# Kernel optimization log

Hardware: AMD Instinct MI355X
Metric: run time of the kernel (lower is better)

The kernel has to match this reference:

```python
import jax, jax.numpy as jnp
import numpy as np

DIM = 1024
HEADS = 16
HEAD_DIM = DIM // HEADS
B, N = 2, 2048


def setup_inputs() -> dict:
    key = jax.random.key(0)
    k1, k2, k3, k4 = jax.random.split(key, 4)
    scale = 1.0 / np.sqrt(DIM)
    return {
        "x": jax.random.normal(k1, (B, N, DIM), dtype=jnp.float32),
        "w_qkv": jax.random.normal(k2, (DIM, 3 * DIM), dtype=jnp.float32) * scale,
        "w_out": jax.random.normal(k3, (DIM, DIM), dtype=jnp.float32) * scale,
        "b_out": jax.random.normal(k4, (DIM,), dtype=jnp.float32) * 0.01,
    }


def reference(x, w_qkv, w_out, b_out):
    b, n, c = x.shape
    h, d = HEADS, c // HEADS
    sm_scale = d ** -0.5
    qkv = x @ w_qkv  # [b, n, 3c]
    q, k, v = jnp.split(qkv, 3, axis=-1)
    # [b, n, c] -> [b, h, n, d]
    q = q.reshape(b, n, h, d).transpose(0, 2, 1, 3)
    k = k.reshape(b, n, h, d).transpose(0, 2, 1, 3)
    v = v.reshape(b, n, h, d).transpose(0, 2, 1, 3)
    dots = jnp.einsum("bhqd,bhkd->bhqk", q, k) * sm_scale
    attn = jax.nn.softmax(dots, axis=-1)
    out = jnp.einsum("bhqk,bhkd->bhqd", attn, v)
    out = out.transpose(0, 2, 1, 3).reshape(b, n, c)
    return out @ w_out + b_out
```

## Files before the change

### kernel.cpp

```cpp
#include <hip/hip_runtime.h>
#include <hip/hip_bf16.h>

typedef __attribute__((ext_vector_type(8))) short bf16x8;
typedef __attribute__((ext_vector_type(4))) float f32x4;

#define B_    2
#define N_    2048
#define DIM_  1024
#define H_    16
#define D_    64
#define BH_   32
#define QSC   0.18033688f

static __device__ __forceinline__ void gload_lds16(const void* g, void* l) {
  __builtin_amdgcn_global_load_lds((const __attribute__((address_space(1))) void*)g,
                                   (__attribute__((address_space(3))) void*)l, 16, 0, 0);
}

__global__ __launch_bounds__(256) void prep_kernel(const float* __restrict__ x,
                                                   const float* __restrict__ w_qkv,
                                                   const float* __restrict__ w_out,
                                                   __hip_bfloat16* __restrict__ xb,
                                                   __hip_bfloat16* __restrict__ wqkT,
                                                   __hip_bfloat16* __restrict__ woT) {
  __shared__ float tile[64][65];
  const int bid = blockIdx.x, t = threadIdx.x;
  if (bid < 4096) {
    const int i = bid * 256 + t;
    float4 v = reinterpret_cast<const float4*>(x)[i];
    union { __hip_bfloat16 h[4]; uint2 u; } cv;
    cv.h[0] = __float2bfloat16(v.x);
    cv.h[1] = __float2bfloat16(v.y);
    cv.h[2] = __float2bfloat16(v.z);
    cv.h[3] = __float2bfloat16(v.w);
    reinterpret_cast<uint2*>(xb)[i] = cv.u;
    return;
  }
  const float* in;
  __hip_bfloat16* out;
  int R, C, c0, r0;
  if (bid < 4096 + 768) {
    const int bx = bid - 4096;
    in = w_qkv; out = wqkT; R = 1024; C = 3072;
    c0 = (bx % 48) * 64; r0 = (bx / 48) * 64;
  } else {
    const int bx = bid - 4096 - 768;
    in = w_out; out = woT; R = 1024; C = 1024;
    c0 = (bx % 16) * 64; r0 = (bx / 16) * 64;
  }
#pragma unroll
  for (int i = 0; i < 16; ++i) {
    int idx = i * 256 + t;
    int r = idx >> 6, c = idx & 63;
    tile[r][c] = in[(size_t)(r0 + r) * C + (c0 + c)];
  }
  __syncthreads();
#pragma unroll
  for (int i = 0; i < 16; ++i) {
    int idx = i * 256 + t;
    int rr = idx >> 6, cc = idx & 63;
    out[(size_t)(c0 + rr) * R + (r0 + cc)] = __float2bfloat16(tile[cc][rr]);
  }
}

__global__ __launch_bounds__(512, 2) void gemm_qkv_kernel(const __hip_bfloat16* __restrict__ A,
                                                          const __hip_bfloat16* __restrict__ Bt,
                                                          __hip_bfloat16* __restrict__ Qw,
                                                          __hip_bfloat16* __restrict__ Kw,
                                                          __hip_bfloat16* __restrict__ Vt) {
  __shared__ __align__(16) char lds[131072];
  const int t = threadIdx.x, w = t >> 6, lane = t & 63;
  const int l16 = lane & 15, kg = lane >> 4;
  int flat = blockIdx.y * 12 + blockIdx.x;
  flat = (flat & 7) * 24 + (flat >> 3);
  const int bx = flat % 12, by = flat / 12;
  const int m0 = by * 256, n0 = bx * 256;
  const int wm = w >> 2, wn = w & 3;
  const int rA = t >> 3;
  const int jb = (t & 7) ^ (rA & 7);

#define LDSOFF(bb, mat) (((bb) * 2 + (mat)) * 32768)
#define STG_A(bb, tt, h)                                                                    \
  do {                                                                                      \
    gload_lds16(A + (size_t)(m0 + rA + 64 * (h)) * 1024 + (tt) * 64 + jb * 8,               \
                (char*)lds + LDSOFF(bb, 0) + (h) * 8192 + t * 16);                          \
    gload_lds16(A + (size_t)(m0 + rA + 64 * (h) + 128) * 1024 + (tt) * 64 + jb * 8,         \
                (char*)lds + LDSOFF(bb, 0) + (h) * 8192 + 16384 + t * 16);                  \
  } while (0)
#define STG_B(bb, tt, h)                                                                    \
  do {                                                                                      \
    gload_lds16(Bt + (size_t)(n0 + rA + 128 * (h)) * 1024 + (tt) * 64 + jb * 8,             \
                (char*)lds + LDSOFF(bb, 1) + (h) * 16384 + t * 16);                         \
    gload_lds16(Bt + (size_t)(n0 + rA + 128 * (h) + 64) * 1024 + (tt) * 64 + jb * 8,        \
                (char*)lds + LDSOFF(bb, 1) + (h) * 16384 + 8192 + t * 16);                  \
  } while (0)
#define RD_A(dst, q, i, kk)                                                                 \
  {                                                                                         \
    const int row = wm * 128 + ((q) * 2 + (i)) * 16 + l16;                                  \
    dst = *reinterpret_cast<const bf16x8*>(Ab + row * 128 + ((((kk) * 4 + kg) ^ (row & 7)) * 16)); \
  }
#define RD_B(dst, nj, kk)                                                                   \
  {                                                                                         \
    const int row = wn * 64 + (nj) * 16 + l16;                                              \
    dst = *reinterpret_cast<const bf16x8*>(Bb + row * 128 + ((((kk) * 4 + kg) ^ (row & 7)) * 16)); \
  }
#define PHASE(q)                                                                            \
  do {                                                                                      \
    bf16x8 af[2][2];                                                                        \
    _Pragma("unroll") for (int i = 0; i < 2; ++i)                                           \
      _Pragma("unroll") for (int kk = 0; kk < 2; ++kk) RD_A(af[i][kk], q, i, kk);           \
    __builtin_amdgcn_s_setprio(1);                                                          \
    _Pragma("unroll") for (int i = 0; i < 2; ++i)                                           \
      _Pragma("unroll") for (int nj = 0; nj < 4; ++nj)                                      \
        _Pragma("unroll") for (int kk = 0; kk < 2; ++kk)                                    \
          acc[(q) * 2 + i][nj] =                                                            \
              __builtin_amdgcn_mfma_f32_16x16x32_bf16(af[i][kk], bfr[nj][kk],               \
                                                      acc[(q) * 2 + i][nj], 0, 0, 0);       \
    __builtin_amdgcn_s_setprio(0);                                                          \
  } while (0)

  f32x4 acc[8][4];
#pragma unroll
  for (int i = 0; i < 8; ++i)
#pragma unroll
    for (int j = 0; j < 4; ++j) acc[i][j] = {0.f, 0.f, 0.f, 0.f};

  STG_A(0, 0, 0); STG_A(0, 0, 1); STG_B(0, 0, 0); STG_B(0, 0, 1);
  STG_B(1, 1, 0); STG_B(1, 1, 1); STG_A(1, 1, 0);

#pragma unroll 1
  for (int kt = 0; kt < 16; ++kt) {
    const int b = kt & 1;
    const char* Ab = (const char*)lds + LDSOFF(b, 0);
    const char* Bb = (const char*)lds + LDSOFF(b, 1);

    if (kt < 15) STG_A(b ^ 1, kt + 1, 1);
    __builtin_amdgcn_sched_barrier(0);
    if (kt < 15) asm volatile("s_waitcnt vmcnt(8)" ::: "memory");
    else         asm volatile("s_waitcnt vmcnt(0)" ::: "memory");
    __builtin_amdgcn_s_barrier();
    __builtin_amdgcn_sched_barrier(0);
    bf16x8 bfr[4][2];
#pragma unroll
    for (int nj = 0; nj < 4; ++nj)
#pragma unroll
      for (int kk = 0; kk < 2; ++kk) RD_B(bfr[nj][kk], nj, kk);
    PHASE(0);
    __builtin_amdgcn_s_barrier();
    __builtin_amdgcn_sched_barrier(0);

    if (kt < 14) STG_B(b, kt + 2, 0);
    __builtin_amdgcn_sched_barrier(0);
    PHASE(1);
    __builtin_amdgcn_s_barrier();
    __builtin_amdgcn_sched_barrier(0);

    if (kt < 14) STG_B(b, kt + 2, 1);
    PHASE(2);

    if (kt < 14) STG_A(b, kt + 2, 0);
    __builtin_amdgcn_sched_barrier(0);
    PHASE(3);
    __builtin_amdgcn_s_barrier();
    __builtin_amdgcn_sched_barrier(0);
  }

  const int which = n0 >> 10;
#pragma unroll
  for (int nj = 0; nj < 4; ++nj) {
    const int n = n0 + wn * 64 + nj * 16 + l16;
    const int nn = n & 1023;
    const int h = nn >> 6, d = nn & 63;
#pragma unroll
    for (int mi = 0; mi < 8; ++mi) {
      const int m = m0 + wm * 128 + mi * 16 + kg * 4;
      const int bb = m >> 11, tt = m & 2047;
      if (which == 2) {
        union { __hip_bfloat16 hh[4]; unsigned long long u; } pv;
#pragma unroll
        for (int r = 0; r < 4; ++r) pv.hh[r] = __float2bfloat16(acc[mi][nj][r]);
        *reinterpret_cast<unsigned long long*>(
            &Vt[((size_t)(bb * H_ + h) * D_ + d) * N_ + tt]) = pv.u;
      } else {
        __hip_bfloat16* dst = (which == 0) ? Qw : Kw;
        const float sc = (which == 0) ? QSC : 1.0f;
#pragma unroll
        for (int r = 0; r < 4; ++r)
          dst[((size_t)(bb * H_ + h) * N_ + tt + r) * D_ + d] = __float2bfloat16(acc[mi][nj][r] * sc);
      }
    }
  }
#undef PHASE
#undef RD_B
#undef RD_A
#undef STG_B
#undef STG_A
#undef LDSOFF
}

__global__ __launch_bounds__(256) void gemm_out_kernel(const __hip_bfloat16* __restrict__ A,
                                                       const __hip_bfloat16* __restrict__ Bt,
                                                       const float* __restrict__ bo,
                                                       float* __restrict__ out) {
  __shared__ __align__(16) char lds[65536];
  const int t = threadIdx.x, w = t >> 6, lane = t & 63;
  const int l16 = lane & 15, kg = lane >> 4;
  const int m0 = blockIdx.y * 128, n0 = blockIdx.x * 128;
  const int wm = w >> 1, wn = w & 1;

  f32x4 acc[4][4];
#pragma unroll
  for (int i = 0; i < 4; ++i)
#pragma unroll
    for (int j = 0; j < 4; ++j) acc[i][j] = {0.f, 0.f, 0.f, 0.f};

  size_t srcA[4], srcB[4];
#pragma unroll
  for (int i = 0; i < 4; ++i) {
    const int c = 256 * i + t;
    const int row = c >> 3, jsw = (c & 7) ^ (row & 7);
    srcA[i] = (size_t)(m0 + row) * 1024 + jsw * 8;
    srcB[i] = (size_t)(n0 + row) * 1024 + jsw * 8;
  }
#define OSTG(bb, k0)                                                          \
  do {                                                                        \
    _Pragma("unroll") for (int i = 0; i < 4; ++i) {                           \
      gload_lds16(A + srcA[i] + (k0), (char*)lds + (bb) * 32768 + i * 4096 + w * 1024);          \
      gload_lds16(Bt + srcB[i] + (k0), (char*)lds + (bb) * 32768 + 16384 + i * 4096 + w * 1024); \
    }                                                                         \
  } while (0)

  OSTG(0, 0);

#pragma unroll 1
  for (int kt = 0; kt < 16; ++kt) {
    const int b = kt & 1;
    __builtin_amdgcn_s_barrier();
    __builtin_amdgcn_sched_barrier(0);
    if (kt + 1 < 16) OSTG(b ^ 1, (kt + 1) * 64);
    __builtin_amdgcn_sched_barrier(0);
    if (kt + 1 < 16) asm volatile("s_waitcnt vmcnt(8)" ::: "memory");
    else             asm volatile("s_waitcnt vmcnt(0)" ::: "memory");
    __builtin_amdgcn_s_barrier();
    __builtin_amdgcn_sched_barrier(0);
    const char* Ab = (const char*)lds + b * 32768;
    const char* Bb = (const char*)lds + b * 32768 + 16384;
#pragma unroll
    for (int kk = 0; kk < 2; ++kk) {
      bf16x8 a[4], bfr[4];
#pragma unroll
      for (int i = 0; i < 4; ++i) {
        const int row = wm * 64 + i * 16 + l16;
        const int jsw = ((kk << 2) | kg) ^ (row & 7);
        a[i] = *reinterpret_cast<const bf16x8*>(Ab + row * 128 + jsw * 16);
      }
#pragma unroll
      for (int j = 0; j < 4; ++j) {
        const int row = wn * 64 + j * 16 + l16;
        const int jsw = ((kk << 2) | kg) ^ (row & 7);
        bfr[j] = *reinterpret_cast<const bf16x8*>(Bb + row * 128 + jsw * 16);
      }
      __builtin_amdgcn_s_setprio(1);
#pragma unroll
      for (int i = 0; i < 4; ++i)
#pragma unroll
        for (int j = 0; j < 4; ++j)
          acc[i][j] = __builtin_amdgcn_mfma_f32_16x16x32_bf16(a[i], bfr[j], acc[i][j], 0, 0, 0);
      __builtin_amdgcn_s_setprio(0);
    }
  }
#undef OSTG

#pragma unroll
  for (int j = 0; j < 4; ++j) {
    const int n = n0 + wn * 64 + j * 16 + l16;
    const float bias = bo[n];
#pragma unroll
    for (int i = 0; i < 4; ++i) {
#pragma unroll
      for (int r = 0; r < 4; ++r) {
        const int m = m0 + wm * 64 + i * 16 + kg * 4 + r;
        out[(size_t)m * 1024 + n] = acc[i][j][r] + bias;
      }
    }
  }
}

__global__ __launch_bounds__(512) void attn_kernel(const __hip_bfloat16* __restrict__ Q,
                                                   const __hip_bfloat16* __restrict__ K,
                                                   const __hip_bfloat16* __restrict__ Vt,
                                                   __hip_bfloat16* __restrict__ O) {
  __shared__ __align__(16) __hip_bfloat16 Ks[3][64 * 64];
  __shared__ __align__(16) __hip_bfloat16 Vs[3][64 * 64];
  __shared__ __align__(16) __hip_bfloat16 Plds[8][16][64];
  const int bh = blockIdx.y;
  const int q0 = blockIdx.x * 128;
  const int t = threadIdx.x, w = t >> 6, lane = t & 63;
  const int l16 = lane & 15, kg = lane >> 4;
  const int b = bh >> 4, h = bh & 15;

  const __hip_bfloat16* Kbh = K + (size_t)bh * N_ * D_;
  const __hip_bfloat16* Vbh = Vt + (size_t)bh * D_ * N_;

  const int crow = t >> 3, cb = t & 7;
  const int csw = cb ^ (crow & 7);
  const size_t offK = (size_t)crow * D_ + csw * 8;
  const size_t offV = (size_t)crow * N_ + csw * 8;

  const __hip_bfloat16* Qp = Q + ((size_t)bh * N_ + q0 + w * 16 + l16) * D_ + kg * 8;
  const bf16x8 qf0 = *reinterpret_cast<const bf16x8*>(Qp);
  const bf16x8 qf1 = *reinterpret_cast<const bf16x8*>(Qp + 32);

  float dacc = 0.f;
  f32x4 oacc[4];
#pragma unroll
  for (int dn = 0; dn < 4; ++dn) oacc[dn] = {0.f, 0.f, 0.f, 0.f};

#define STAGE(bufi, kv)                                                          \
  do {                                                                           \
    gload_lds16(Kbh + (size_t)(kv) * D_ + offK, (char*)Ks[bufi] + w * 1024);     \
    gload_lds16(Vbh + (kv) + offV,              (char*)Vs[bufi] + w * 1024);     \
  } while (0)

  STAGE(0, 0);
  STAGE(1, 64);

#pragma unroll 1
  for (int it = 0; it < N_ / 64; ++it) {
    if (it < N_ / 64 - 1) asm volatile("s_waitcnt vmcnt(2)" ::: "memory");
    else                  asm volatile("s_waitcnt vmcnt(0)" ::: "memory");
    __builtin_amdgcn_s_barrier();
    __builtin_amdgcn_sched_barrier(0);
    if (it + 2 < N_ / 64) STAGE((it + 2) % 3, (it + 2) * 64);
    __builtin_amdgcn_sched_barrier(0);

    const char* Kb = (const char*)Ks[it % 3];
    const char* Vb = (const char*)Vs[it % 3];

    f32x4 s[4];
#pragma unroll
    for (int kt = 0; kt < 4; ++kt) s[kt] = {0.f, 0.f, 0.f, 0.f};
    __builtin_amdgcn_s_setprio(1);
#pragma unroll
    for (int kt = 0; kt < 4; ++kt) {
      const int row = kt * 16 + l16;
      const int rsw = (row & 7) << 4;
      const bf16x8 k0 = *reinterpret_cast<const bf16x8*>(Kb + row * 128 + ((kg << 4) ^ rsw));
      const bf16x8 k1 = *reinterpret_cast<const bf16x8*>(Kb + row * 128 + (((4 + kg) << 4) ^ rsw));
      s[kt] = __builtin_amdgcn_mfma_f32_16x16x32_bf16(k0, qf0, s[kt], 0, 0, 0);
      s[kt] = __builtin_amdgcn_mfma_f32_16x16x32_bf16(k1, qf1, s[kt], 0, 0, 0);
    }
    __builtin_amdgcn_s_setprio(0);

    const int xm3 = (l16 & 7) << 3;
    float ds = 0.f;
#pragma unroll
    for (int kt = 0; kt < 4; ++kt) {
      const float p0 = __builtin_amdgcn_exp2f(s[kt][0]);
      const float p1 = __builtin_amdgcn_exp2f(s[kt][1]);
      const float p2 = __builtin_amdgcn_exp2f(s[kt][2]);
      const float p3 = __builtin_amdgcn_exp2f(s[kt][3]);
      ds += (p0 + p1) + (p2 + p3);
      union { __hip_bfloat162 h2[2]; unsigned long long u; } pk;
      pk.h2[0] = __float22bfloat162_rn(make_float2(p0, p1));
      pk.h2[1] = __float22bfloat162_rn(make_float2(p2, p3));
      *reinterpret_cast<unsigned long long*>(&Plds[w][l16][(16 * kt + 4 * kg) ^ xm3]) = pk.u;
    }
    dacc += ds;

    __builtin_amdgcn_s_setprio(1);
#pragma unroll
    for (int kk = 0; kk < 2; ++kk) {
      const bf16x8 pa = *reinterpret_cast<const bf16x8*>(
          &Plds[w][l16][(kk * 32 + kg * 8) ^ xm3]);
#pragma unroll
      for (int dn = 0; dn < 4; ++dn) {
        const int vrow = dn * 16 + l16;
        const int vsw = (vrow & 7) << 4;
        const bf16x8 vf = *reinterpret_cast<const bf16x8*>(
            Vb + vrow * 128 + ((kk * 64 + kg * 16) ^ vsw));
        oacc[dn] = __builtin_amdgcn_mfma_f32_16x16x32_bf16(pa, vf, oacc[dn], 0, 0, 0);
      }
    }
    __builtin_amdgcn_s_setprio(0);
  }
#undef STAGE

  float dtot = dacc + __shfl_xor(dacc, 16);
  dtot += __shfl_xor(dtot, 32);
  float inv[4];
#pragma unroll
  for (int r = 0; r < 4; ++r) inv[r] = 1.0f / __shfl(dtot, kg * 4 + r);

  __hip_bfloat16* Ob = O + ((size_t)b * N_ + q0 + w * 16) * DIM_ + h * D_;
#pragma unroll
  for (int dn = 0; dn < 4; ++dn)
#pragma unroll
    for (int r = 0; r < 4; ++r)
      Ob[(size_t)(kg * 4 + r) * DIM_ + dn * 16 + l16] = __float2bfloat16(oacc[dn][r] * inv[r]);
}

extern "C" void kernel_launch(void* const* d_in, const int* in_sizes, int n_in,
                              void* d_out, int out_size, void* d_ws, size_t ws_size,
                              hipStream_t stream) {
  const float* x = (const float*)d_in[0];
  const float* w_qkv = (const float*)d_in[1];
  const float* w_out = (const float*)d_in[2];
  const float* b_out = (const float*)d_in[3];
  float* out = (float*)d_out;

  __hip_bfloat16* ws = (__hip_bfloat16*)d_ws;
  __hip_bfloat16* xb = ws;
  __hip_bfloat16* wqkT = xb + (size_t)4096 * 1024;
  __hip_bfloat16* woT = wqkT + (size_t)3072 * 1024;
  __hip_bfloat16* Qw = woT + (size_t)1024 * 1024;
  __hip_bfloat16* Kw = Qw + (size_t)BH_ * N_ * D_;
  __hip_bfloat16* Vt = Kw + (size_t)BH_ * N_ * D_;
  __hip_bfloat16* Ow = Vt + (size_t)BH_ * N_ * D_;

  prep_kernel<<<5120, 256, 0, stream>>>(x, w_qkv, w_out, xb, wqkT, woT);
  gemm_qkv_kernel<<<dim3(12, 16), 512, 0, stream>>>(xb, wqkT, Qw, Kw, Vt);
  attn_kernel<<<dim3(16, 32), 512, 0, stream>>>(Qw, Kw, Vt, Ow);
  gemm_out_kernel<<<dim3(8, 32), 256, 0, stream>>>(Ow, woT, b_out, out);
}
```

Before: 116.3 us.

## Split attention KV loop across two wave groups with 32-row Q per wave

Each wave now handles 32 query rows, so every K fragment read from LDS feeds two Q tiles. The eight waves split into two groups that process alternating KV tiles out of a four-deep LDS ring, and their partial outputs are merged through LDS at the end. The softmax denominator is now computed with an MFMA against a ones vector instead of scalar adds plus shuffles. This adds an end-of-kernel reduction, a larger LDS footprint that may limit occupancy, and a full vmcnt(0) wait on every iteration.

```diff
diff --git a/kernel.cpp b/kernel.cpp
--- a/kernel.cpp
+++ b/kernel.cpp
@@ -286,18 +286,18 @@
   }
 }
 
-__global__ __launch_bounds__(512) void attn_kernel(const __hip_bfloat16* __restrict__ Q,
-                                                   const __hip_bfloat16* __restrict__ K,
-                                                   const __hip_bfloat16* __restrict__ Vt,
-                                                   __hip_bfloat16* __restrict__ O) {
-  __shared__ __align__(16) __hip_bfloat16 Ks[3][64 * 64];
-  __shared__ __align__(16) __hip_bfloat16 Vs[3][64 * 64];
-  __shared__ __align__(16) __hip_bfloat16 Plds[8][16][64];
+__global__ __launch_bounds__(512, 4) void attn_kernel(const __hip_bfloat16* __restrict__ Q,
+                                                      const __hip_bfloat16* __restrict__ K,
+                                                      const __hip_bfloat16* __restrict__ Vt,
+                                                      __hip_bfloat16* __restrict__ O) {
+  __shared__ __align__(16) char lds[81920];
   const int bh = blockIdx.y;
   const int q0 = blockIdx.x * 128;
   const int t = threadIdx.x, w = t >> 6, lane = t & 63;
   const int l16 = lane & 15, kg = lane >> 4;
   const int b = bh >> 4, h = bh & 15;
+  const int grp = w >> 2;
+  const int qbase = q0 + (w & 3) * 32;
 
   const __hip_bfloat16* Kbh = K + (size_t)bh * N_ * D_;
   const __hip_bfloat16* Vbh = Vt + (size_t)bh * D_ * N_;
@@ -307,39 +307,58 @@
   const size_t offK = (size_t)crow * D_ + csw * 8;
   const size_t offV = (size_t)crow * N_ + csw * 8;
 
-  const __hip_bfloat16* Qp = Q + ((size_t)bh * N_ + q0 + w * 16 + l16) * D_ + kg * 8;
-  const bf16x8 qf0 = *reinterpret_cast<const bf16x8*>(Qp);
-  const bf16x8 qf1 = *reinterpret_cast<const bf16x8*>(Qp + 32);
-
-  float dacc = 0.f;
-  f32x4 oacc[4];
-#pragma unroll
-  for (int dn = 0; dn < 4; ++dn) oacc[dn] = {0.f, 0.f, 0.f, 0.f};
-
-#define STAGE(bufi, kv)                                                          \
-  do {                                                                           \
-    gload_lds16(Kbh + (size_t)(kv) * D_ + offK, (char*)Ks[bufi] + w * 1024);     \
-    gload_lds16(Vbh + (kv) + offV,              (char*)Vs[bufi] + w * 1024);     \
+  bf16x8 qf[2][2];
+#pragma unroll
+  for (int qh = 0; qh < 2; ++qh) {
+    const __hip_bfloat16* Qrow = Q + ((size_t)bh * N_ + qbase + 16 * qh + l16) * D_ + kg * 8;
+    qf[qh][0] = *reinterpret_cast<const bf16x8*>(Qrow);
+    qf[qh][1] = *reinterpret_cast<const bf16x8*>(Qrow + 32);
+  }
+
+  bf16x8 ones;
+#pragma unroll
+  for (int i = 0; i < 8; ++i) ones[i] = (short)0x3F80;
+
+  f32x4 oaccS[2];
+  f32x4 oacc[2][4];
+#pragma unroll
+  for (int qh = 0; qh < 2; ++qh) {
+    oaccS[qh] = {0.f, 0.f, 0.f, 0.f};
+#pragma unroll
+    for (int dn = 0; dn < 4; ++dn) oacc[qh][dn] = {0.f, 0.f, 0.f, 0.f};
+  }
+
+  char* Plw = lds + 65536 + w * 2048;
+
+#define STAGE(bufi, kv)                                                            \
+  do {                                                                             \
+    gload_lds16(Kbh + (size_t)(kv) * D_ + offK, lds + (bufi) * 16384 + w * 1024);  \
+    gload_lds16(Vbh + (kv) + offV, lds + (bufi) * 16384 + 8192 + w * 1024);        \
   } while (0)
 
   STAGE(0, 0);
   STAGE(1, 64);
 
 #pragma unroll 1
-  for (int it = 0; it < N_ / 64; ++it) {
-    if (it < N_ / 64 - 1) asm volatile("s_waitcnt vmcnt(2)" ::: "memory");
-    else                  asm volatile("s_waitcnt vmcnt(0)" ::: "memory");
-    __builtin_amdgcn_s_barrier();
-    __builtin_amdgcn_sched_barrier(0);
-    if (it + 2 < N_ / 64) STAGE((it + 2) % 3, (it + 2) * 64);
-    __builtin_amdgcn_sched_barrier(0);
-
-    const char* Kb = (const char*)Ks[it % 3];
-    const char* Vb = (const char*)Vs[it % 3];
-
-    f32x4 s[4];
-#pragma unroll
-    for (int kt = 0; kt < 4; ++kt) s[kt] = {0.f, 0.f, 0.f, 0.f};
+  for (int p = 0; p < 16; ++p) {
+    asm volatile("s_waitcnt vmcnt(0)" ::: "memory");
+    __builtin_amdgcn_s_barrier();
+    __builtin_amdgcn_sched_barrier(0);
+    if (p < 15) {
+      STAGE((2 * p + 2) & 3, (2 * p + 2) * 64);
+      STAGE((2 * p + 3) & 3, (2 * p + 3) * 64);
+    }
+    __builtin_amdgcn_sched_barrier(0);
+
+    const int myt = 2 * p + grp;
+    const char* Kb = lds + (myt & 3) * 16384;
+    const char* Vb = Kb + 8192;
+
+    f32x4 s[2][4];
+#pragma unroll
+    for (int qh = 0; qh < 2; ++qh)
+#pragma unroll
+      for (int kt = 0; kt < 4; ++kt) s[qh][kt] = {0.f, 0.f, 0.f, 0.f};
     __builtin_amdgcn_s_setprio(1);
 #pragma unroll
     for (int kt = 0; kt < 4; ++kt) {
@@ -347,57 +366,81 @@
       const int rsw = (row & 7) << 4;
       const bf16x8 k0 = *reinterpret_cast<const bf16x8*>(Kb + row * 128 + ((kg << 4) ^ rsw));
       const bf16x8 k1 = *reinterpret_cast<const bf16x8*>(Kb + row * 128 + (((4 + kg) << 4) ^ rsw));
-      s[kt] = __builtin_amdgcn_mfma_f32_16x16x32_bf16(k0, qf0, s[kt], 0, 0, 0);
-      s[kt] = __builtin_amdgcn_mfma_f32_16x16x32_bf16(k1, qf1, s[kt], 0, 0, 0);
+      s[0][kt] = __builtin_amdgcn_mfma_f32_16x16x32_bf16(k0, qf[0][0], s[0][kt], 0, 0, 0);
+      s[0][kt] = __builtin_amdgcn_mfma_f32_16x16x32_bf16(k1, qf[0][1], s[0][kt], 0, 0, 0);
+      s[1][kt] = __builtin_amdgcn_mfma_f32_16x16x32_bf16(k0, qf[1][0], s[1][kt], 0, 0, 0);
+      s[1][kt] = __builtin_amdgcn_mfma_f32_16x16x32_bf16(k1, qf[1][1], s[1][kt], 0, 0, 0);
     }
     __builtin_amdgcn_s_setprio(0);
 
     const int xm3 = (l16 & 7) << 3;
-    float ds = 0.f;
-#pragma unroll
-    for (int kt = 0; kt < 4; ++kt) {
-      const float p0 = __builtin_amdgcn_exp2f(s[kt][0]);
-      const float p1 = __builtin_amdgcn_exp2f(s[kt][1]);
-      const float p2 = __builtin_amdgcn_exp2f(s[kt][2]);
-      const float p3 = __builtin_amdgcn_exp2f(s[kt][3]);
-      ds += (p0 + p1) + (p2 + p3);
-      union { __hip_bfloat162 h2[2]; unsigned long long u; } pk;
-      pk.h2[0] = __float22bfloat162_rn(make_float2(p0, p1));
-      pk.h2[1] = __float22bfloat162_rn(make_float2(p2, p3));
-      *reinterpret_cast<unsigned long long*>(&Plds[w][l16][(16 * kt + 4 * kg) ^ xm3]) = pk.u;
-    }
-    dacc += ds;
-
-    __builtin_amdgcn_s_setprio(1);
-#pragma unroll
-    for (int kk = 0; kk < 2; ++kk) {
-      const bf16x8 pa = *reinterpret_cast<const bf16x8*>(
-          &Plds[w][l16][(kk * 32 + kg * 8) ^ xm3]);
-#pragma unroll
-      for (int dn = 0; dn < 4; ++dn) {
-        const int vrow = dn * 16 + l16;
-        const int vsw = (vrow & 7) << 4;
-        const bf16x8 vf = *reinterpret_cast<const bf16x8*>(
-            Vb + vrow * 128 + ((kk * 64 + kg * 16) ^ vsw));
-        oacc[dn] = __builtin_amdgcn_mfma_f32_16x16x32_bf16(pa, vf, oacc[dn], 0, 0, 0);
-      }
-    }
-    __builtin_amdgcn_s_setprio(0);
+#pragma unroll
+    for (int qh = 0; qh < 2; ++qh) {
+#pragma unroll
+      for (int kt = 0; kt < 4; ++kt) {
+        union { __hip_bfloat162 h2[2]; unsigned long long u; } pk;
+        pk.h2[0] = __float22bfloat162_rn(make_float2(__builtin_amdgcn_exp2f(s[qh][kt][0]),
+                                                     __builtin_amdgcn_exp2f(s[qh][kt][1])));
+        pk.h2[1] = __float22bfloat162_rn(make_float2(__builtin_amdgcn_exp2f(s[qh][kt][2]),
+                                                     __builtin_amdgcn_exp2f(s[qh][kt][3])));
+        *reinterpret_cast<unsigned long long*>(
+            Plw + l16 * 128 + ((16 * kt + 4 * kg) ^ xm3) * 2) = pk.u;
+      }
+      __builtin_amdgcn_s_setprio(1);
+#pragma unroll
+      for (int kk = 0; kk < 2; ++kk) {
+        const bf16x8 pa = *reinterpret_cast<const bf16x8*>(
+            Plw + l16 * 128 + ((kk * 32 + kg * 8) ^ xm3) * 2);
+        oaccS[qh] = __builtin_amdgcn_mfma_f32_16x16x32_bf16(pa, ones, oaccS[qh], 0, 0, 0);
+#pragma unroll
+        for (int dn = 0; dn < 4; ++dn) {
+          const int vrow = dn * 16 + l16;
+          const int vsw = (vrow & 7) << 4;
+          const bf16x8 vf = *reinterpret_cast<const bf16x8*>(
+              Vb + vrow * 128 + ((kk * 64 + kg * 16) ^ vsw));
+          oacc[qh][dn] = __builtin_amdgcn_mfma_f32_16x16x32_bf16(pa, vf, oacc[qh][dn], 0, 0, 0);
+        }
+      }
+      __builtin_amdgcn_s_setprio(0);
+      __builtin_amdgcn_sched_barrier(0);
+    }
   }
 #undef STAGE
 
-  float dtot = dacc + __shfl_xor(dacc, 16);
-  dtot += __shfl_xor(dtot, 32);
-  float inv[4];
-#pragma unroll
-  for (int r = 0; r < 4; ++r) inv[r] = 1.0f / __shfl(dtot, kg * 4 + r);
-
-  __hip_bfloat16* Ob = O + ((size_t)b * N_ + q0 + w * 16) * DIM_ + h * D_;
-#pragma unroll
-  for (int dn = 0; dn < 4; ++dn)
-#pragma unroll
-    for (int r = 0; r < 4; ++r)
-      Ob[(size_t)(kg * 4 + r) * DIM_ + dn * 16 + l16] = __float2bfloat16(oacc[dn][r] * inv[r]);
+  __syncthreads();
+  float* red = (float*)lds;
+  if (grp == 1) {
+    const int wp = w - 4;
+#pragma unroll
+    for (int qh = 0; qh < 2; ++qh) {
+#pragma unroll
+      for (int dn = 0; dn < 4; ++dn)
+#pragma unroll
+        for (int r = 0; r < 4; ++r)
+          red[(qh * 16 + dn * 4 + r) * 256 + wp * 64 + lane] = oacc[qh][dn][r];
+#pragma unroll
+      for (int r = 0; r < 4; ++r)
+        red[(32 + qh * 4 + r) * 256 + wp * 64 + lane] = oaccS[qh][r];
+    }
+  }
+  __syncthreads();
+  if (grp == 0) {
+#pragma unroll
+    for (int qh = 0; qh < 2; ++qh) {
+      float inv[4];
+#pragma unroll
+      for (int r = 0; r < 4; ++r)
+        inv[r] = 1.0f / (oaccS[qh][r] + red[(32 + qh * 4 + r) * 256 + w * 64 + lane]);
+      __hip_bfloat16* Ob = O + ((size_t)b * N_ + qbase + 16 * qh) * DIM_ + h * D_;
+#pragma unroll
+      for (int dn = 0; dn < 4; ++dn)
+#pragma unroll
+        for (int r = 0; r < 4; ++r) {
+          const float v = (oacc[qh][dn][r] + red[(qh * 16 + dn * 4 + r) * 256 + w * 64 + lane]) * inv[r];
+          Ob[(size_t)(kg * 4 + r) * DIM_ + dn * 16 + l16] = __float2bfloat16(v);
+        }
+    }
+  }
 }
 
 extern "C" void kernel_launch(void* const* d_in, const int* in_sizes, int n_in,
```

New measurement: 111.4 us. 1.04x faster.

## Process two KV tiles per barrier and compute softmax row sums with MFMA

Applied to the files above, without the earlier changes.

The attention loop now handles two 64-key tiles per iteration from a double-buffered 64 KB LDS region, replacing the three-stage single-tile ring. This halves the number of barriers and waitcnts per key. The softmax denominator is now accumulated by an MFMA of P against a ones vector instead of VALU adds and cross-lane shuffles, so the sum uses the same bf16-rounded P as the numerator. Launch bounds now request occupancy 4, which caps registers per thread; the larger 80 KB LDS footprint may limit how many blocks fit on each CU.

```diff
diff --git a/kernel.cpp b/kernel.cpp
--- a/kernel.cpp
+++ b/kernel.cpp
@@ -286,13 +286,11 @@
   }
 }
 
-__global__ __launch_bounds__(512) void attn_kernel(const __hip_bfloat16* __restrict__ Q,
-                                                   const __hip_bfloat16* __restrict__ K,
-                                                   const __hip_bfloat16* __restrict__ Vt,
-                                                   __hip_bfloat16* __restrict__ O) {
-  __shared__ __align__(16) __hip_bfloat16 Ks[3][64 * 64];
-  __shared__ __align__(16) __hip_bfloat16 Vs[3][64 * 64];
-  __shared__ __align__(16) __hip_bfloat16 Plds[8][16][64];
+__global__ __launch_bounds__(512, 4) void attn_kernel(const __hip_bfloat16* __restrict__ Q,
+                                                      const __hip_bfloat16* __restrict__ K,
+                                                      const __hip_bfloat16* __restrict__ Vt,
+                                                      __hip_bfloat16* __restrict__ O) {
+  __shared__ __align__(16) char lds[81920];
   const int bh = blockIdx.y;
   const int q0 = blockIdx.x * 128;
   const int t = threadIdx.x, w = t >> 6, lane = t & 63;
@@ -311,87 +309,128 @@
   const bf16x8 qf0 = *reinterpret_cast<const bf16x8*>(Qp);
   const bf16x8 qf1 = *reinterpret_cast<const bf16x8*>(Qp + 32);
 
-  float dacc = 0.f;
+  bf16x8 ones;
+#pragma unroll
+  for (int i = 0; i < 8; ++i) ones[i] = (short)0x3F80;
+
+  f32x4 oaccS = {0.f, 0.f, 0.f, 0.f};
   f32x4 oacc[4];
 #pragma unroll
   for (int dn = 0; dn < 4; ++dn) oacc[dn] = {0.f, 0.f, 0.f, 0.f};
 
-#define STAGE(bufi, kv)                                                          \
-  do {                                                                           \
-    gload_lds16(Kbh + (size_t)(kv) * D_ + offK, (char*)Ks[bufi] + w * 1024);     \
-    gload_lds16(Vbh + (kv) + offV,              (char*)Vs[bufi] + w * 1024);     \
-  } while (0)
-
-  STAGE(0, 0);
-  STAGE(1, 64);
+  char* Plw = lds + 65536 + w * 2048;
+
+#define STAGE1(base, kv)                                                \
+  do {                                                                  \
+    gload_lds16(Kbh + (size_t)(kv) * D_ + offK, (base) + w * 1024);     \
+    gload_lds16(Vbh + (kv) + offV, (base) + 8192 + w * 1024);           \
+  } while (0)
+#define STAGEP(pb, kv0)                                                 \
+  do {                                                                  \
+    STAGE1(lds + (pb) * 32768, kv0);                                    \
+    STAGE1(lds + (pb) * 32768 + 16384, (kv0) + 64);                     \
+  } while (0)
+
+  STAGEP(0, 0);
+  asm volatile("s_waitcnt vmcnt(0)" ::: "memory");
+  __builtin_amdgcn_s_barrier();
 
 #pragma unroll 1
-  for (int it = 0; it < N_ / 64; ++it) {
-    if (it < N_ / 64 - 1) asm volatile("s_waitcnt vmcnt(2)" ::: "memory");
-    else                  asm volatile("s_waitcnt vmcnt(0)" ::: "memory");
-    __builtin_amdgcn_s_barrier();
-    __builtin_amdgcn_sched_barrier(0);
-    if (it + 2 < N_ / 64) STAGE((it + 2) % 3, (it + 2) * 64);
-    __builtin_amdgcn_sched_barrier(0);
-
-    const char* Kb = (const char*)Ks[it % 3];
-    const char* Vb = (const char*)Vs[it % 3];
-
-    f32x4 s[4];
-#pragma unroll
-    for (int kt = 0; kt < 4; ++kt) s[kt] = {0.f, 0.f, 0.f, 0.f};
+  for (int p = 0; p < 16; ++p) {
+    if (p < 15) STAGEP((p + 1) & 1, (2 * p + 2) * 64);
+    __builtin_amdgcn_sched_barrier(0);
+
+    const char* base = lds + (p & 1) * 32768;
+    const char* Kb0 = base;
+    const char* Vb0 = base + 8192;
+    const char* Kb1 = base + 16384;
+    const char* Vb1 = base + 24576;
+
+    f32x4 s0[4], s1[4];
+#pragma unroll
+    for (int kt = 0; kt < 4; ++kt) { s0[kt] = {0.f, 0.f, 0.f, 0.f}; s1[kt] = {0.f, 0.f, 0.f, 0.f}; }
     __builtin_amdgcn_s_setprio(1);
 #pragma unroll
     for (int kt = 0; kt < 4; ++kt) {
       const int row = kt * 16 + l16;
       const int rsw = (row & 7) << 4;
-      const bf16x8 k0 = *reinterpret_cast<const bf16x8*>(Kb + row * 128 + ((kg << 4) ^ rsw));
-      const bf16x8 k1 = *reinterpret_cast<const bf16x8*>(Kb + row * 128 + (((4 + kg) << 4) ^ rsw));
-      s[kt] = __builtin_amdgcn_mfma_f32_16x16x32_bf16(k0, qf0, s[kt], 0, 0, 0);
-      s[kt] = __builtin_amdgcn_mfma_f32_16x16x32_bf16(k1, qf1, s[kt], 0, 0, 0);
+      const int o0 = (kg << 4) ^ rsw, o1 = ((4 + kg) << 4) ^ rsw;
+      const bf16x8 ka0 = *reinterpret_cast<const bf16x8*>(Kb0 + row * 128 + o0);
+      const bf16x8 ka1 = *reinterpret_cast<const bf16x8*>(Kb0 + row * 128 + o1);
+      const bf16x8 kb0 = *reinterpret_cast<const bf16x8*>(Kb1 + row * 128 + o0);
+      const bf16x8 kb1 = *reinterpret_cast<const bf16x8*>(Kb1 + row * 128 + o1);
+      s0[kt] = __builtin_amdgcn_mfma_f32_16x16x32_bf16(ka0, qf0, s0[kt], 0, 0, 0);
+      s0[kt] = __builtin_amdgcn_mfma_f32_16x16x32_bf16(ka1, qf1, s0[kt], 0, 0, 0);
+      s1[kt] = __builtin_amdgcn_mfma_f32_16x16x32_bf16(kb0, qf0, s1[kt], 0, 0, 0);
+      s1[kt] = __builtin_amdgcn_mfma_f32_16x16x32_bf16(kb1, qf1, s1[kt], 0, 0, 0);
     }
     __builtin_amdgcn_s_setprio(0);
 
     const int xm3 = (l16 & 7) << 3;
-    float ds = 0.f;
+
 #pragma unroll
     for (int kt = 0; kt < 4; ++kt) {
-      const float p0 = __builtin_amdgcn_exp2f(s[kt][0]);
-      const float p1 = __builtin_amdgcn_exp2f(s[kt][1]);
-      const float p2 = __builtin_amdgcn_exp2f(s[kt][2]);
-      const float p3 = __builtin_amdgcn_exp2f(s[kt][3]);
-      ds += (p0 + p1) + (p2 + p3);
       union { __hip_bfloat162 h2[2]; unsigned long long u; } pk;
-      pk.h2[0] = __float22bfloat162_rn(make_float2(p0, p1));
-      pk.h2[1] = __float22bfloat162_rn(make_float2(p2, p3));
-      *reinterpret_cast<unsigned long long*>(&Plds[w][l16][(16 * kt + 4 * kg) ^ xm3]) = pk.u;
-    }
-    dacc += ds;
-
+      pk.h2[0] = __float22bfloat162_rn(make_float2(__builtin_amdgcn_exp2f(s0[kt][0]),
+                                                   __builtin_amdgcn_exp2f(s0[kt][1])));
+      pk.h2[1] = __float22bfloat162_rn(make_float2(__builtin_amdgcn_exp2f(s0[kt][2]),
+                                                   __builtin_amdgcn_exp2f(s0[kt][3])));
+      *reinterpret_cast<unsigned long long*>(
+          Plw + l16 * 128 + (((16 * kt + 4 * kg) ^ xm3) << 1)) = pk.u;
+    }
     __builtin_amdgcn_s_setprio(1);
 #pragma unroll
     for (int kk = 0; kk < 2; ++kk) {
       const bf16x8 pa = *reinterpret_cast<const bf16x8*>(
-          &Plds[w][l16][(kk * 32 + kg * 8) ^ xm3]);
+          Plw + l16 * 128 + (((kk * 32 + kg * 8) ^ xm3) << 1));
+      oaccS = __builtin_amdgcn_mfma_f32_16x16x32_bf16(pa, ones, oaccS, 0, 0, 0);
 #pragma unroll
       for (int dn = 0; dn < 4; ++dn) {
         const int vrow = dn * 16 + l16;
         const int vsw = (vrow & 7) << 4;
         const bf16x8 vf = *reinterpret_cast<const bf16x8*>(
-            Vb + vrow * 128 + ((kk * 64 + kg * 16) ^ vsw));
+            Vb0 + vrow * 128 + ((kk * 64 + kg * 16) ^ vsw));
         oacc[dn] = __builtin_amdgcn_mfma_f32_16x16x32_bf16(pa, vf, oacc[dn], 0, 0, 0);
       }
     }
     __builtin_amdgcn_s_setprio(0);
-  }
-#undef STAGE
-
-  float dtot = dacc + __shfl_xor(dacc, 16);
-  dtot += __shfl_xor(dtot, 32);
+
+#pragma unroll
+    for (int kt = 0; kt < 4; ++kt) {
+      union { __hip_bfloat162 h2[2]; unsigned long long u; } pk;
+      pk.h2[0] = __float22bfloat162_rn(make_float2(__builtin_amdgcn_exp2f(s1[kt][0]),
+                                                   __builtin_amdgcn_exp2f(s1[kt][1])));
+      pk.h2[1] = __float22bfloat162_rn(make_float2(__builtin_amdgcn_exp2f(s1[kt][2]),
+                                                   __builtin_amdgcn_exp2f(s1[kt][3])));
+      *reinterpret_cast<unsigned long long*>(
+          Plw + l16 * 128 + (((16 * kt + 4 * kg) ^ xm3) << 1)) = pk.u;
+    }
+    __builtin_amdgcn_s_setprio(1);
+#pragma unroll
+    for (int kk = 0; kk < 2; ++kk) {
+      const bf16x8 pa = *reinterpret_cast<const bf16x8*>(
+          Plw + l16 * 128 + (((kk * 32 + kg * 8) ^ xm3) << 1));
+      oaccS = __builtin_amdgcn_mfma_f32_16x16x32_bf16(pa, ones, oaccS, 0, 0, 0);
+#pragma unroll
+      for (int dn = 0; dn < 4; ++dn) {
+        const int vrow = dn * 16 + l16;
+        const int vsw = (vrow & 7) << 4;
+        const bf16x8 vf = *reinterpret_cast<const bf16x8*>(
+            Vb1 + vrow * 128 + ((kk * 64 + kg * 16) ^ vsw));
+        oacc[dn] = __builtin_amdgcn_mfma_f32_16x16x32_bf16(pa, vf, oacc[dn], 0, 0, 0);
+      }
+    }
+    __builtin_amdgcn_s_setprio(0);
+
+    asm volatile("s_waitcnt vmcnt(0)" ::: "memory");
+    __builtin_amdgcn_s_barrier();
+  }
+#undef STAGEP
+#undef STAGE1
+
   float inv[4];
 #pragma unroll
-  for (int r = 0; r < 4; ++r) inv[r] = 1.0f / __shfl(dtot, kg * 4 + r);
-
+  for (int r = 0; r < 4; ++r) inv[r] = 1.0f / oaccS[r];
   __hip_bfloat16* Ob = O + ((size_t)b * N_ + q0 + w * 16) * DIM_ + h * D_;
 #pragma unroll
   for (int dn = 0; dn < 4; ++dn)
```

Result: faster. 111.9 us (-3.8%).

## Load K directly to registers, double-buffer V, compute row sums via MFMA

Applied to the files above, without the earlier changes.

The attention kernel no longer stages K through LDS. Each lane loads its K fragments straight from global memory into registers, ping-ponging between two register sets, while V moves from a triple to a double LDS buffer. The softmax denominator is now computed by an extra MFMA against a vector of ones instead of scalar adds and cross-lane shuffles, and launch bounds ask for 4 blocks per SM. This trims LDS traffic and footprint to raise occupancy, at the cost of more VGPRs, uncoalesced direct global K loads, and a full vmcnt(0) wait plus a barrier on every tile.

```diff
diff --git a/kernel.cpp b/kernel.cpp
--- a/kernel.cpp
+++ b/kernel.cpp
@@ -286,12 +286,11 @@
   }
 }
 
-__global__ __launch_bounds__(512) void attn_kernel(const __hip_bfloat16* __restrict__ Q,
-                                                   const __hip_bfloat16* __restrict__ K,
-                                                   const __hip_bfloat16* __restrict__ Vt,
-                                                   __hip_bfloat16* __restrict__ O) {
-  __shared__ __align__(16) __hip_bfloat16 Ks[3][64 * 64];
-  __shared__ __align__(16) __hip_bfloat16 Vs[3][64 * 64];
+__global__ __launch_bounds__(512, 4) void attn_kernel(const __hip_bfloat16* __restrict__ Q,
+                                                      const __hip_bfloat16* __restrict__ K,
+                                                      const __hip_bfloat16* __restrict__ Vt,
+                                                      __hip_bfloat16* __restrict__ O) {
+  __shared__ __align__(16) __hip_bfloat16 Vs[2][64 * 64];
   __shared__ __align__(16) __hip_bfloat16 Plds[8][16][64];
   const int bh = blockIdx.y;
   const int q0 = blockIdx.x * 128;
@@ -304,94 +303,95 @@
 
   const int crow = t >> 3, cb = t & 7;
   const int csw = cb ^ (crow & 7);
-  const size_t offK = (size_t)crow * D_ + csw * 8;
   const size_t offV = (size_t)crow * N_ + csw * 8;
 
   const __hip_bfloat16* Qp = Q + ((size_t)bh * N_ + q0 + w * 16 + l16) * D_ + kg * 8;
   const bf16x8 qf0 = *reinterpret_cast<const bf16x8*>(Qp);
   const bf16x8 qf1 = *reinterpret_cast<const bf16x8*>(Qp + 32);
 
-  float dacc = 0.f;
+  const __hip_bfloat16* Kln = Kbh + (size_t)l16 * D_ + kg * 8;
+
+  bf16x8 ones;
+#pragma unroll
+  for (int i = 0; i < 8; ++i) ones[i] = (short)0x3F80;
+
+  f32x4 oaccS = {0.f, 0.f, 0.f, 0.f};
   f32x4 oacc[4];
 #pragma unroll
   for (int dn = 0; dn < 4; ++dn) oacc[dn] = {0.f, 0.f, 0.f, 0.f};
 
-#define STAGE(bufi, kv)                                                          \
-  do {                                                                           \
-    gload_lds16(Kbh + (size_t)(kv) * D_ + offK, (char*)Ks[bufi] + w * 1024);     \
-    gload_lds16(Vbh + (kv) + offV,              (char*)Vs[bufi] + w * 1024);     \
-  } while (0)
-
-  STAGE(0, 0);
-  STAGE(1, 64);
+#define STAGE_V(bufi, kv) gload_lds16(Vbh + (kv) + offV, (char*)Vs[bufi] + w * 1024)
+#define KLOAD(dst, kv)                                                                  \
+  do {                                                                                  \
+    _Pragma("unroll") for (int kt_ = 0; kt_ < 4; ++kt_) {                               \
+      dst##0[kt_] = *reinterpret_cast<const bf16x8*>(Kln + (size_t)((kv) + kt_ * 16) * D_);        \
+      dst##1[kt_] = *reinterpret_cast<const bf16x8*>(Kln + (size_t)((kv) + kt_ * 16) * D_ + 32);   \
+    }                                                                                   \
+  } while (0)
+
+  bf16x8 kA0[4], kA1[4], kB0[4], kB1[4];
+
+  STAGE_V(0, 0);
+  KLOAD(kA, 0);
+  asm volatile("s_waitcnt vmcnt(0)" ::: "memory");
+  __builtin_amdgcn_s_barrier();
+
+  const int xm3 = (l16 & 7) << 3;
+
+#define TILE_BODY(e, KF0, KF1, KN)                                                      \
+  do {                                                                                  \
+    const int nxt = (e) + 1;                                                            \
+    if (nxt < 32) STAGE_V(nxt & 1, nxt * 64);                                           \
+    KLOAD(KN, (nxt < 32 ? nxt : 31) * 64);                                              \
+    __builtin_amdgcn_sched_barrier(0);                                                  \
+    const char* Vb = (const char*)Vs[(e) & 1];                                          \
+    f32x4 s[4];                                                                         \
+    _Pragma("unroll") for (int kt = 0; kt < 4; ++kt) s[kt] = {0.f, 0.f, 0.f, 0.f};      \
+    __builtin_amdgcn_s_setprio(1);                                                      \
+    _Pragma("unroll") for (int kt = 0; kt < 4; ++kt) {                                  \
+      s[kt] = __builtin_amdgcn_mfma_f32_16x16x32_bf16(KF0[kt], qf0, s[kt], 0, 0, 0);    \
+      s[kt] = __builtin_amdgcn_mfma_f32_16x16x32_bf16(KF1[kt], qf1, s[kt], 0, 0, 0);    \
+    }                                                                                   \
+    __builtin_amdgcn_s_setprio(0);                                                      \
+    _Pragma("unroll") for (int kt = 0; kt < 4; ++kt) {                                  \
+      union { __hip_bfloat162 h2[2]; unsigned long long u; } pk;                        \
+      pk.h2[0] = __float22bfloat162_rn(make_float2(__builtin_amdgcn_exp2f(s[kt][0]),    \
+                                                   __builtin_amdgcn_exp2f(s[kt][1])));  \
+      pk.h2[1] = __float22bfloat162_rn(make_float2(__builtin_amdgcn_exp2f(s[kt][2]),    \
+                                                   __builtin_amdgcn_exp2f(s[kt][3])));  \
+      *reinterpret_cast<unsigned long long*>(                                           \
+          &Plds[w][l16][(16 * kt + 4 * kg) ^ xm3]) = pk.u;                              \
+    }                                                                                   \
+    __builtin_amdgcn_s_setprio(1);                                                      \
+    _Pragma("unroll") for (int kk = 0; kk < 2; ++kk) {                                  \
+      const bf16x8 pa = *reinterpret_cast<const bf16x8*>(                               \
+          &Plds[w][l16][(kk * 32 + kg * 8) ^ xm3]);                                     \
+      oaccS = __builtin_amdgcn_mfma_f32_16x16x32_bf16(pa, ones, oaccS, 0, 0, 0);        \
+      _Pragma("unroll") for (int dn = 0; dn < 4; ++dn) {                                \
+        const int vrow = dn * 16 + l16;                                                 \
+        const int vsw = (vrow & 7) << 4;                                                \
+        const bf16x8 vf = *reinterpret_cast<const bf16x8*>(                             \
+            Vb + vrow * 128 + ((kk * 64 + kg * 16) ^ vsw));                             \
+        oacc[dn] = __builtin_amdgcn_mfma_f32_16x16x32_bf16(pa, vf, oacc[dn], 0, 0, 0);  \
+      }                                                                                 \
+    }                                                                                   \
+    __builtin_amdgcn_s_setprio(0);                                                      \
+    asm volatile("s_waitcnt vmcnt(0)" ::: "memory");                                    \
+    __builtin_amdgcn_s_barrier();                                                       \
+  } while (0)
 
 #pragma unroll 1
-  for (int it = 0; it < N_ / 64; ++it) {
-    if (it < N_ / 64 - 1) asm volatile("s_waitcnt vmcnt(2)" ::: "memory");
-    else                  asm volatile("s_waitcnt vmcnt(0)" ::: "memory");
-    __builtin_amdgcn_s_barrier();
-    __builtin_amdgcn_sched_barrier(0);
-    if (it + 2 < N_ / 64) STAGE((it + 2) % 3, (it + 2) * 64);
-    __builtin_amdgcn_sched_barrier(0);
-
-    const char* Kb = (const char*)Ks[it % 3];
-    const char* Vb = (const char*)Vs[it % 3];
-
-    f32x4 s[4];
-#pragma unroll
-    for (int kt = 0; kt < 4; ++kt) s[kt] = {0.f, 0.f, 0.f, 0.f};
-    __builtin_amdgcn_s_setprio(1);
-#pragma unroll
-    for (int kt = 0; kt < 4; ++kt) {
-      const int row = kt * 16 + l16;
-      const int rsw = (row & 7) << 4;
-      const bf16x8 k0 = *reinterpret_cast<const bf16x8*>(Kb + row * 128 + ((kg << 4) ^ rsw));
-      const bf16x8 k1 = *reinterpret_cast<const bf16x8*>(Kb + row * 128 + (((4 + kg) << 4) ^ rsw));
-      s[kt] = __builtin_amdgcn_mfma_f32_16x16x32_bf16(k0, qf0, s[kt], 0, 0, 0);
-      s[kt] = __builtin_amdgcn_mfma_f32_16x16x32_bf16(k1, qf1, s[kt], 0, 0, 0);
-    }
-    __builtin_amdgcn_s_setprio(0);
-
-    const int xm3 = (l16 & 7) << 3;
-    float ds = 0.f;
-#pragma unroll
-    for (int kt = 0; kt < 4; ++kt) {
-      const float p0 = __builtin_amdgcn_exp2f(s[kt][0]);
-      const float p1 = __builtin_amdgcn_exp2f(s[kt][1]);
-      const float p2 = __builtin_amdgcn_exp2f(s[kt][2]);
-      const float p3 = __builtin_amdgcn_exp2f(s[kt][3]);
-      ds += (p0 + p1) + (p2 + p3);
-      union { __hip_bfloat162 h2[2]; unsigned long long u; } pk;
-      pk.h2[0] = __float22bfloat162_rn(make_float2(p0, p1));
-      pk.h2[1] = __float22bfloat162_rn(make_float2(p2, p3));
-      *reinterpret_cast<unsigned long long*>(&Plds[w][l16][(16 * kt + 4 * kg) ^ xm3]) = pk.u;
-    }
-    dacc += ds;
-
-    __builtin_amdgcn_s_setprio(1);
-#pragma unroll
-    for (int kk = 0; kk < 2; ++kk) {
-      const bf16x8 pa = *reinterpret_cast<const bf16x8*>(
-          &Plds[w][l16][(kk * 32 + kg * 8) ^ xm3]);
-#pragma unroll
-      for (int dn = 0; dn < 4; ++dn) {
-        const int vrow = dn * 16 + l16;
-        const int vsw = (vrow & 7) << 4;
-        const bf16x8 vf = *reinterpret_cast<const bf16x8*>(
-            Vb + vrow * 128 + ((kk * 64 + kg * 16) ^ vsw));
-        oacc[dn] = __builtin_amdgcn_mfma_f32_16x16x32_bf16(pa, vf, oacc[dn], 0, 0, 0);
-      }
-    }
-    __builtin_amdgcn_s_setprio(0);
-  }
-#undef STAGE
-
-  float dtot = dacc + __shfl_xor(dacc, 16);
-  dtot += __shfl_xor(dtot, 32);
+  for (int p = 0; p < 16; ++p) {
+    TILE_BODY(2 * p,     kA0, kA1, kB);
+    TILE_BODY(2 * p + 1, kB0, kB1, kA);
+  }
+#undef TILE_BODY
+#undef KLOAD
+#undef STAGE_V
+
   float inv[4];
 #pragma unroll
-  for (int r = 0; r < 4; ++r) inv[r] = 1.0f / __shfl(dtot, kg * 4 + r);
-
+  for (int r = 0; r < 4; ++r) inv[r] = 1.0f / oaccS[r];
   __hip_bfloat16* Ob = O + ((size_t)b * N_ + q0 + w * 16) * DIM_ + h * D_;
 #pragma unroll
   for (int dn = 0; dn < 4; ++dn)
```

Measured after the change: 189.8 us. 1.63x slower.
